# Performance work log

Hardware: AMD Instinct MI355X
Metric: run time of the kernel (lower is better)

## Reference

```python
import jax, jax.numpy as jnp
import numpy as np
import math

NUM_HEADS = 16
KEY_DIM = 64
MODEL_DIM = 1024
NEG_INF = -1000000000.0


def _get_slopes(n):
    def pow2_slopes(n):
        start = 2 ** (-2 ** (-(math.log2(n) - 3)))
        return [start * start ** i for i in range(n)]
    if math.log2(n).is_integer():
        s = pow2_slopes(n)
    else:
        c = 2 ** math.floor(math.log2(n))
        s = pow2_slopes(c) + pow2_slopes(2 * c)[0::2][: n - c]
    return jnp.asarray(s, dtype=jnp.float32)


def setup_inputs() -> dict:
    key = jax.random.key(0)
    ks = jax.random.split(key, 11)
    B, S, D = 4, 2048, MODEL_DIM
    P = NUM_HEADS * KEY_DIM
    sd = 1.0 / math.sqrt(D)
    return {
        "query": jax.random.normal(ks[0], (B, S, D), jnp.float32),
        "key": jax.random.normal(ks[1], (B, S, D), jnp.float32),
        "value": jax.random.normal(ks[2], (B, S, D), jnp.float32),
        "Wq": jax.random.normal(ks[3], (D, P), jnp.float32) * sd,
        "bq": jnp.zeros((P,), jnp.float32),
        "Wk": jax.random.normal(ks[4], (D, P), jnp.float32) * sd,
        "bk": jnp.zeros((P,), jnp.float32),
        "Wv": jax.random.normal(ks[5], (D, P), jnp.float32) * sd,
        "bv": jnp.zeros((P,), jnp.float32),
        "Wo": jax.random.normal(ks[6], (P, D), jnp.float32) * (1.0 / math.sqrt(P)),
        "bo": jnp.zeros((D,), jnp.float32),
    }


def reference(query, key, value, Wq, bq, Wk, bk, Wv, bv, Wo, bo):
    B, S, _ = query.shape
    H, Kd = NUM_HEADS, KEY_DIM

    def split_heads(x):  # [B,S,H*Kd] -> [B,H,S,Kd]
        return x.reshape(B, S, H, Kd).transpose(0, 2, 1, 3)

    q = split_heads(query @ Wq + bq)
    k = split_heads(key @ Wk + bk)
    v = split_heads(value @ Wv + bv)

    logits = jnp.einsum("bhqd,bhkd->bhqk", q, k) / jnp.sqrt(jnp.float32(Kd))

    i = jnp.arange(S)[:, None]
    j = jnp.arange(S)[None, :]
    causal = jnp.where(i >= j, 0.0, NEG_INF).astype(jnp.float32)  # [S,S]
    rel = (i - j).astype(jnp.float32)  # [S,S]
    slopes = _get_slopes(H)  # [H]
    alibi = slopes[:, None, None] * rel  # [H,S,S]
    logits = logits + causal[None, None, :, :] + alibi[None, :, :, :]

    weights = jax.nn.softmax(logits, axis=-1)
    attn = jnp.einsum("bhqk,bhkd->bhqd", weights, v)
    concat = attn.transpose(0, 2, 1, 3).reshape(B, S, H * Kd)
    return concat @ Wo + bo
```

## Files before the change

kernel.cpp:

```cpp
#include <hip/hip_runtime.h>

#define B_ 4
#define S_ 2048
#define D_ 1024
#define H_ 16
#define KD_ 64
#define P_ 1024
#define M_ (B_*S_)

typedef unsigned short u16;
typedef unsigned int u32;
typedef __attribute__((ext_vector_type(4))) float f32x4;
typedef __attribute__((ext_vector_type(8))) __bf16 bf16x8;

__device__ __forceinline__ u16 f2bf(float f) {
  u32 x = __float_as_uint(f);
  return (u16)((x + 0x7fffu + ((x >> 16) & 1u)) >> 16);
}

__device__ __forceinline__ void gl_lds16(const u16* g, u16* l) {
  __builtin_amdgcn_global_load_lds((__attribute__((address_space(1))) void*)g,
                                   (__attribute__((address_space(3))) void*)l, 16, 0, 0);
}

__device__ __forceinline__ u32 pkbf(float a, float b) {
  return __builtin_amdgcn_perm(__float_as_uint(b) + 0x8000u,
                               __float_as_uint(a) + 0x8000u, 0x07060302u);
}

__global__ void cvt3_kernel(const float* __restrict__ q, const float* __restrict__ k,
                            const float* __restrict__ v,
                            u16* __restrict__ Xq, u16* __restrict__ Xk, u16* __restrict__ Xv) {
  const int z = blockIdx.y;
  const float* in = z == 0 ? q : z == 1 ? k : v;
  u16* out = z == 0 ? Xq : z == 1 ? Xk : Xv;
  int i = blockIdx.x * 256 + threadIdx.x;
  float4 vv = ((const float4*)in)[i];
  ((u32*)out)[i*2+0] = (u32)f2bf(vv.x) | ((u32)f2bf(vv.y) << 16);
  ((u32*)out)[i*2+1] = (u32)f2bf(vv.z) | ((u32)f2bf(vv.w) << 16);
}

__global__ void transpose_cvt4(const float* __restrict__ Wq, const float* __restrict__ Wk,
                               const float* __restrict__ Wv, const float* __restrict__ Wo,
                               u16* __restrict__ WqT, u16* __restrict__ WkT,
                               u16* __restrict__ WvT, u16* __restrict__ WoT) {
  const int z = blockIdx.z;
  const float* in = z == 0 ? Wq : z == 1 ? Wk : z == 2 ? Wv : Wo;
  u16* out = z == 0 ? WqT : z == 1 ? WkT : z == 2 ? WvT : WoT;
  __shared__ float tile[32][33];
  int bx = blockIdx.x * 32, by = blockIdx.y * 32;
  int tx = threadIdx.x, ty = threadIdx.y;
  #pragma unroll
  for (int kk = 0; kk < 4; ++kk)
    tile[ty + kk*8][tx] = in[(by + ty + kk*8) * 1024 + bx + tx];
  __syncthreads();
  #pragma unroll
  for (int kk = 0; kk < 4; ++kk)
    out[(bx + ty + kk*8) * 1024 + by + tx] = f2bf(tile[tx][ty + kk*8]);
}

__global__ __launch_bounds__(256) void gemm_qkv(
    const u16* __restrict__ Xq, const u16* __restrict__ Xk, const u16* __restrict__ Xv,
    const u16* __restrict__ WqT, const u16* __restrict__ WkT, const u16* __restrict__ WvT,
    const float* __restrict__ bq, const float* __restrict__ bk, const float* __restrict__ bv,
    u16* __restrict__ Qb, u16* __restrict__ Kb, u16* __restrict__ Vt)
{
  constexpr int K = 1024, N = 1024, BK = 32;
  const int z = blockIdx.z;
  const u16* A  = z == 0 ? Xq  : z == 1 ? Xk  : Xv;
  const u16* Bt = z == 0 ? WqT : z == 1 ? WkT : WvT;
  const float* bias = z == 0 ? bq : z == 1 ? bk : bv;

  __shared__ alignas(16) u16 As[128*BK];
  __shared__ alignas(16) u16 Bs[128*BK];
  const int tid = threadIdx.x;
  const int w = tid >> 6, l = tid & 63;
  const int quad = l >> 4, l16 = l & 15;
  const int wm = (w >> 1) * 64, wn = (w & 1) * 64;
  const long mBase = (long)blockIdx.x * 128;
  const int  nBase = blockIdx.y * 128;

  f32x4 acc[4][4] = {};
  const int off0 = w*1024 + l*16;

  for (int kb = 0; kb < K/BK; ++kb) {
    __syncthreads();
    #pragma unroll
    for (int p = 0; p < 2; ++p) {
      int off = p*4096 + off0;
      int row = off >> 6;
      int cb  = off & 63;
      const u16* ga = A  + (mBase + row)*K + kb*BK + (cb >> 1);
      const u16* gb = Bt + ((long)(nBase + row))*K + kb*BK + (cb >> 1);
      gl_lds16(ga, (u16*)((char*)As + p*4096 + w*1024));
      gl_lds16(gb, (u16*)((char*)Bs + p*4096 + w*1024));
    }
    __syncthreads();
    bf16x8 af[4], bf[4];
    #pragma unroll
    for (int i = 0; i < 4; ++i) af[i] = *(const bf16x8*)&As[(wm + i*16 + l16)*BK + quad*8];
    #pragma unroll
    for (int j = 0; j < 4; ++j) bf[j] = *(const bf16x8*)&Bs[(wn + j*16 + l16)*BK + quad*8];
    #pragma unroll
    for (int i = 0; i < 4; ++i)
      #pragma unroll
      for (int j = 0; j < 4; ++j)
        acc[i][j] = __builtin_amdgcn_mfma_f32_16x16x32_bf16(af[i], bf[j], acc[i][j], 0, 0, 0);
  }

  if (z < 2) {
    u16* Cout = z == 0 ? Qb : Kb;
    #pragma unroll
    for (int i = 0; i < 4; ++i)
      #pragma unroll
      for (int j = 0; j < 4; ++j)
        #pragma unroll
        for (int r = 0; r < 4; ++r) {
          long row = mBase + wm + i*16 + quad*4 + r;
          int  col = nBase + wn + j*16 + l16;
          Cout[row*N + col] = f2bf(acc[i][j][r] + bias[col]);
        }
  } else {
    #pragma unroll
    for (int i = 0; i < 4; ++i)
      #pragma unroll
      for (int j = 0; j < 4; ++j) {
        int  col  = nBase + wn + j*16 + l16;
        long row0 = mBase + wm + i*16 + quad*4;
        int  bb = (int)(row0 >> 11);
        int  ss = (int)(row0 & 2047);
        float bcol = bias[col];
        float v0 = acc[i][j][0] + bcol, v1 = acc[i][j][1] + bcol;
        float v2 = acc[i][j][2] + bcol, v3 = acc[i][j][3] + bcol;
        uint2 pk;
        pk.x = (u32)f2bf(v0) | ((u32)f2bf(v1) << 16);
        pk.y = (u32)f2bf(v2) | ((u32)f2bf(v3) << 16);
        *(uint2*)&Vt[((long)(bb*16) * 64 + col) * 2048 + ss] = pk;
      }
  }
}

__global__ __launch_bounds__(256) void gemm_out(const u16* __restrict__ A,
                                                const u16* __restrict__ Bt,
                                                const float* __restrict__ bias,
                                                float* __restrict__ Cout)
{
  constexpr int K = 1024, N = 1024, BK = 32;
  __shared__ alignas(16) u16 As[128*BK];
  __shared__ alignas(16) u16 Bs[128*BK];
  const int tid = threadIdx.x;
  const int w = tid >> 6, l = tid & 63;
  const int quad = l >> 4, l16 = l & 15;
  const int wm = (w >> 1) * 64, wn = (w & 1) * 64;
  const long mBase = (long)blockIdx.x * 128;
  const int  nBase = blockIdx.y * 128;

  f32x4 acc[4][4] = {};
  const int off0 = w*1024 + l*16;

  for (int kb = 0; kb < K/BK; ++kb) {
    __syncthreads();
    #pragma unroll
    for (int p = 0; p < 2; ++p) {
      int off = p*4096 + off0;
      int row = off >> 6;
      int cb  = off & 63;
      const u16* ga = A  + (mBase + row)*K + kb*BK + (cb >> 1);
      const u16* gb = Bt + ((long)(nBase + row))*K + kb*BK + (cb >> 1);
      gl_lds16(ga, (u16*)((char*)As + p*4096 + w*1024));
      gl_lds16(gb, (u16*)((char*)Bs + p*4096 + w*1024));
    }
    __syncthreads();
    bf16x8 af[4], bf[4];
    #pragma unroll
    for (int i = 0; i < 4; ++i) af[i] = *(const bf16x8*)&As[(wm + i*16 + l16)*BK + quad*8];
    #pragma unroll
    for (int j = 0; j < 4; ++j) bf[j] = *(const bf16x8*)&Bs[(wn + j*16 + l16)*BK + quad*8];
    #pragma unroll
    for (int i = 0; i < 4; ++i)
      #pragma unroll
      for (int j = 0; j < 4; ++j)
        acc[i][j] = __builtin_amdgcn_mfma_f32_16x16x32_bf16(af[i], bf[j], acc[i][j], 0, 0, 0);
  }

  #pragma unroll
  for (int i = 0; i < 4; ++i)
    #pragma unroll
    for (int j = 0; j < 4; ++j)
      #pragma unroll
      for (int r = 0; r < 4; ++r) {
        long row = mBase + wm + i*16 + quad*4 + r;
        int  col = nBase + wn + j*16 + l16;
        Cout[row*N + col] = acc[i][j][r] + bias[col];
      }
}

#define PST 136
__global__ __launch_bounds__(64, 3) void attn_kernel(const u16* __restrict__ Qb,
                                                     const u16* __restrict__ Kb,
                                                     const u16* __restrict__ Vt,
                                                     u16* __restrict__ Ob)
{
  const int n = blockIdx.x;
  const int qt = 15 - (n >> 8);
  const int r8 = n & 255;
  const int b = r8 >> 6, h = (r8 >> 2) & 15, w = r8 & 3;
  const int l = threadIdx.x;
  const int quad = l >> 4, l16 = l & 15;
  const float LOG2E = 1.44269504089f;
  const float slope = exp2f(-0.5f * (float)(h + 1));
  const float c1  = 0.125f * LOG2E;
  const float sl2 = slope * LOG2E;

  __shared__ alignas(16) u16 Ps[2][16][PST];

  const int q0 = qt*128 + w*32;
  const u16* Qp = Qb + ((long)(b*S_ + q0))*P_ + h*KD_;
  const u16* Kp = Kb + ((long)(b*S_))*P_ + h*KD_;
  const u16* Vp = Vt + ((long)(b*H_ + h))*KD_*S_;

  bf16x8 qf[2][2];
  #pragma unroll
  for (int i = 0; i < 2; ++i)
    #pragma unroll
    for (int kk = 0; kk < 2; ++kk)
      qf[i][kk] = *(const bf16x8*)&Qp[(long)(i*16 + l16)*P_ + kk*32 + quad*8];

  f32x4 o[2][4] = {};
  float lsum[2] = {0.f, 0.f};
  const float rs1 = sl2, rs2 = 2.f*sl2, rs3 = 3.f*sl2;

  for (int kt = 0; kt < qt; ++kt) {
    const u16* kts = Kp + (long)(kt*128 + l16)*P_;
    #pragma unroll
    for (int jh = 0; jh < 2; ++jh) {
      f32x4 st[2][4];
      #pragma unroll
      for (int jj = 0; jj < 4; ++jj) {
        const int j = jh*4 + jj;
        const u16* kp = kts + (long)(j*16)*P_;
        bf16x8 kf0 = *(const bf16x8*)(kp + quad*8);
        bf16x8 kf1 = *(const bf16x8*)(kp + 32 + quad*8);
        #pragma unroll
        for (int i = 0; i < 2; ++i) {
          f32x4 t = {};
          t = __builtin_amdgcn_mfma_f32_16x16x32_bf16(kf0, qf[i][0], t, 0, 0, 0);
          t = __builtin_amdgcn_mfma_f32_16x16x32_bf16(kf1, qf[i][1], t, 0, 0, 0);
          st[i][jj] = t;
        }
      }
      #pragma unroll
      for (int i = 0; i < 2; ++i)
        #pragma unroll
        for (int jj = 0; jj < 4; ++jj) {
          const int j = jh*4 + jj;
          const float kb  = (float)(kt*128 + j*16 + quad*4);
          const float bij = -sl2 * kb;
          float p0 = __builtin_amdgcn_exp2f(fmaf(st[i][jj][0], c1, bij));
          float p1 = __builtin_amdgcn_exp2f(fmaf(st[i][jj][1], c1, bij) - rs1);
          float p2 = __builtin_amdgcn_exp2f(fmaf(st[i][jj][2], c1, bij) - rs2);
          float p3 = __builtin_amdgcn_exp2f(fmaf(st[i][jj][3], c1, bij) - rs3);
          lsum[i] += (p0 + p1) + (p2 + p3);
          uint2 pk; pk.x = pkbf(p0, p1); pk.y = pkbf(p2, p3);
          *(uint2*)&Ps[i][l16][j*16 + quad*4] = pk;
        }
    }
    #pragma unroll
    for (int ks = 0; ks < 4; ++ks) {
      bf16x8 pb0 = *(const bf16x8*)&Ps[0][l16][ks*32 + quad*8];
      bf16x8 pb1 = *(const bf16x8*)&Ps[1][l16][ks*32 + quad*8];
      #pragma unroll
      for (int jn = 0; jn < 4; ++jn) {
        bf16x8 vf = *(const bf16x8*)&Vp[(long)(jn*16 + l16)*S_ + kt*128 + ks*32 + quad*8];
        o[0][jn] = __builtin_amdgcn_mfma_f32_16x16x32_bf16(vf, pb0, o[0][jn], 0, 0, 0);
        o[1][jn] = __builtin_amdgcn_mfma_f32_16x16x32_bf16(vf, pb1, o[1][jn], 0, 0, 0);
      }
    }
  }

  {
    const int kt = qt;
    const int jmax = 2*w + 2, ksmax = w + 1;
    const u16* kts = Kp + (long)(kt*128 + l16)*P_;
    for (int j = 0; j < jmax; ++j) {
      const u16* kp = kts + (long)(j*16)*P_;
      bf16x8 kf0 = *(const bf16x8*)(kp + quad*8);
      bf16x8 kf1 = *(const bf16x8*)(kp + 32 + quad*8);
      const int kl0 = j*16 + quad*4;
      const float kb  = (float)(kt*128 + kl0);
      #pragma unroll
      for (int i = 0; i < 2; ++i) {
        f32x4 t = {};
        t = __builtin_amdgcn_mfma_f32_16x16x32_bf16(kf0, qf[i][0], t, 0, 0, 0);
        t = __builtin_amdgcn_mfma_f32_16x16x32_bf16(kf1, qf[i][1], t, 0, 0, 0);
        const int ql = w*32 + i*16 + l16;
        const float bij = -sl2 * kb;
        float x0 = fmaf(t[0], c1, bij);
        float x1 = fmaf(t[1], c1, bij) - rs1;
        float x2 = fmaf(t[2], c1, bij) - rs2;
        float x3 = fmaf(t[3], c1, bij) - rs3;
        if (kl0 + 0 > ql) x0 = -1e30f;
        if (kl0 + 1 > ql) x1 = -1e30f;
        if (kl0 + 2 > ql) x2 = -1e30f;
        if (kl0 + 3 > ql) x3 = -1e30f;
        float p0 = __builtin_amdgcn_exp2f(x0);
        float p1 = __builtin_amdgcn_exp2f(x1);
        float p2 = __builtin_amdgcn_exp2f(x2);
        float p3 = __builtin_amdgcn_exp2f(x3);
        lsum[i] += (p0 + p1) + (p2 + p3);
        uint2 pk; pk.x = pkbf(p0, p1); pk.y = pkbf(p2, p3);
        *(uint2*)&Ps[i][l16][j*16 + quad*4] = pk;
      }
    }
    for (int ks = 0; ks < ksmax; ++ks) {
      bf16x8 pb0 = *(const bf16x8*)&Ps[0][l16][ks*32 + quad*8];
      bf16x8 pb1 = *(const bf16x8*)&Ps[1][l16][ks*32 + quad*8];
      #pragma unroll
      for (int jn = 0; jn < 4; ++jn) {
        bf16x8 vf = *(const bf16x8*)&Vp[(long)(jn*16 + l16)*S_ + kt*128 + ks*32 + quad*8];
        o[0][jn] = __builtin_amdgcn_mfma_f32_16x16x32_bf16(vf, pb0, o[0][jn], 0, 0, 0);
        o[1][jn] = __builtin_amdgcn_mfma_f32_16x16x32_bf16(vf, pb1, o[1][jn], 0, 0, 0);
      }
    }
  }

  #pragma unroll
  for (int i = 0; i < 2; ++i) {
    lsum[i] += __shfl_xor(lsum[i], 16, 64);
    lsum[i] += __shfl_xor(lsum[i], 32, 64);
    const float inv = 1.0f / lsum[i];
    #pragma unroll
    for (int jn = 0; jn < 4; ++jn) {
      float v0 = o[i][jn][0] * inv, v1 = o[i][jn][1] * inv;
      float v2 = o[i][jn][2] * inv, v3 = o[i][jn][3] * inv;
      uint2 pk;
      pk.x = (u32)f2bf(v0) | ((u32)f2bf(v1) << 16);
      pk.y = (u32)f2bf(v2) | ((u32)f2bf(v3) << 16);
      *(uint2*)&Ob[((long)(b*S_ + q0 + i*16 + l16))*P_ + h*KD_ + jn*16 + quad*4] = pk;
    }
  }
}

extern "C" void kernel_launch(void* const* d_in, const int* in_sizes, int n_in,
                              void* d_out, int out_size, void* d_ws, size_t ws_size,
                              hipStream_t stream) {
  const float* q  = (const float*)d_in[0];
  const float* k  = (const float*)d_in[1];
  const float* v  = (const float*)d_in[2];
  const float* Wq = (const float*)d_in[3];
  const float* bq = (const float*)d_in[4];
  const float* Wk = (const float*)d_in[5];
  const float* bk = (const float*)d_in[6];
  const float* Wv = (const float*)d_in[7];
  const float* bv = (const float*)d_in[8];
  const float* Wo = (const float*)d_in[9];
  const float* bo = (const float*)d_in[10];

  const size_t X_ELEMS = (size_t)M_ * P_;
  const size_t W_ELEMS = (size_t)D_ * P_;
  u16* ws  = (u16*)d_ws;
  u16* Xq  = ws;
  u16* Xk  = Xq  + X_ELEMS;
  u16* Xv  = Xk  + X_ELEMS;
  u16* WqT = Xv  + X_ELEMS;
  u16* WkT = WqT + W_ELEMS;
  u16* WvT = WkT + W_ELEMS;
  u16* WoT = WvT + W_ELEMS;
  u16* Qb  = WoT + W_ELEMS;
  u16* Kb  = Qb  + X_ELEMS;
  u16* Vt  = Kb  + X_ELEMS;
  u16* Attn = Xq;

  cvt3_kernel<<<dim3((unsigned)(X_ELEMS/4/256), 3), 256, 0, stream>>>(q, k, v, Xq, Xk, Xv);

  transpose_cvt4<<<dim3(32, 32, 4), dim3(32, 8), 0, stream>>>(Wq, Wk, Wv, Wo,
                                                              WqT, WkT, WvT, WoT);

  gemm_qkv<<<dim3(M_/128, P_/128, 3), 256, 0, stream>>>(Xq, Xk, Xv, WqT, WkT, WvT,
                                                        bq, bk, bv, Qb, Kb, Vt);

  attn_kernel<<<dim3(4096), 64, 0, stream>>>(Qb, Kb, Vt, Attn);

  gemm_out<<<dim3(M_/128, P_/128), 256, 0, stream>>>(Attn, WoT, bo, (float*)d_out);
}
```

Measured before the change: 404.8 us.

## Split attention work into balanced pairs with partial-sum combine kernel

The attention kernel now pairs a long causal q-tile with a short one. Each block handles either the first half of the long tile's key range, or the rest of the long tile plus the whole short tile, so every block does roughly equal work. Partial unnormalized outputs and row sums for the long tiles go to a workspace buffer, and a new combine kernel adds them and normalizes. This works without rescaling because the softmax has no running max. The cost is extra global traffic for the partials, plus one more launch. Launch bounds also rise to allow more resident waves.

```diff
diff --git a/kernel.cpp b/kernel.cpp
--- a/kernel.cpp
+++ b/kernel.cpp
@@ -196,41 +196,26 @@
 }
 
 #define PST 136
-__global__ __launch_bounds__(64, 3) void attn_kernel(const u16* __restrict__ Qb,
-                                                     const u16* __restrict__ Kb,
-                                                     const u16* __restrict__ Vt,
-                                                     u16* __restrict__ Ob)
+__device__ __forceinline__ void attn_tiles(
+    const u16* __restrict__ Qp, const u16* __restrict__ Kp, const u16* __restrict__ Vp,
+    int kt0, int ktN, int qt, bool dodiag, int w, int l16, int quad,
+    float sl2, float c1, u16 (*Ps)[16][PST], f32x4 (&o)[2][4], float (&lsum)[2])
 {
-  const int n = blockIdx.x;
-  const int qt = 15 - (n >> 8);
-  const int r8 = n & 255;
-  const int b = r8 >> 6, h = (r8 >> 2) & 15, w = r8 & 3;
-  const int l = threadIdx.x;
-  const int quad = l >> 4, l16 = l & 15;
-  const float LOG2E = 1.44269504089f;
-  const float slope = exp2f(-0.5f * (float)(h + 1));
-  const float c1  = 0.125f * LOG2E;
-  const float sl2 = slope * LOG2E;
-
-  __shared__ alignas(16) u16 Ps[2][16][PST];
-
-  const int q0 = qt*128 + w*32;
-  const u16* Qp = Qb + ((long)(b*S_ + q0))*P_ + h*KD_;
-  const u16* Kp = Kb + ((long)(b*S_))*P_ + h*KD_;
-  const u16* Vp = Vt + ((long)(b*H_ + h))*KD_*S_;
-
+  const float rs1 = sl2, rs2 = 2.f*sl2, rs3 = 3.f*sl2;
   bf16x8 qf[2][2];
   #pragma unroll
   for (int i = 0; i < 2; ++i)
     #pragma unroll
     for (int kk = 0; kk < 2; ++kk)
       qf[i][kk] = *(const bf16x8*)&Qp[(long)(i*16 + l16)*P_ + kk*32 + quad*8];
-
-  f32x4 o[2][4] = {};
-  float lsum[2] = {0.f, 0.f};
-  const float rs1 = sl2, rs2 = 2.f*sl2, rs3 = 3.f*sl2;
-
-  for (int kt = 0; kt < qt; ++kt) {
+  #pragma unroll
+  for (int i = 0; i < 2; ++i) {
+    lsum[i] = 0.f;
+    #pragma unroll
+    for (int jn = 0; jn < 4; ++jn) o[i][jn] = (f32x4){0.f, 0.f, 0.f, 0.f};
+  }
+
+  for (int kt = kt0; kt < ktN; ++kt) {
     const u16* kts = Kp + (long)(kt*128 + l16)*P_;
     #pragma unroll
     for (int jh = 0; jh < 2; ++jh) {
@@ -278,7 +263,7 @@
     }
   }
 
-  {
+  if (dodiag) {
     const int kt = qt;
     const int jmax = 2*w + 2, ksmax = w + 1;
     const u16* kts = Kp + (long)(kt*128 + l16)*P_;
@@ -323,12 +308,107 @@
       }
     }
   }
-
+}
+
+__global__ __launch_bounds__(64, 4) void attn_kernel(const u16* __restrict__ Qb,
+                                                     const u16* __restrict__ Kb,
+                                                     const u16* __restrict__ Vt,
+                                                     u16* __restrict__ Ob,
+                                                     float* __restrict__ Part)
+{
+  __shared__ alignas(16) u16 Ps[2][16][PST];
+  const int n = blockIdx.x;
+  const int p  = n >> 9;
+  const int ab = (n >> 8) & 1;
+  const int r8 = n & 255;
+  const int b = r8 >> 6, h = (r8 >> 2) & 15, w = r8 & 3;
+  const int qt_hi = 15 - p, qt_lo = p;
+  const int l = threadIdx.x;
+  const int quad = l >> 4, l16 = l & 15;
+  const float LOG2E = 1.44269504089f;
+  const float slope = exp2f(-0.5f * (float)(h + 1));
+  const float c1  = 0.125f * LOG2E;
+  const float sl2 = slope * LOG2E;
+
+  const u16* Kp = Kb + ((long)(b*S_))*P_ + h*KD_;
+  const u16* Vp = Vt + ((long)(b*H_ + h))*KD_*S_;
+  const int slot = ((p*4 + w)*4 + b)*16 + h;
+
+  f32x4 o[2][4];
+  float lsum[2];
+
+  if (ab == 0) {
+    const int q0 = qt_hi*128 + w*32;
+    attn_tiles(Qb + ((long)(b*S_ + q0))*P_ + h*KD_, Kp, Vp,
+               0, 8, qt_hi, false, w, l16, quad, sl2, c1, Ps, o, lsum);
+    float* dst = Part + ((long)slot*64 + l)*36;
+    #pragma unroll
+    for (int i = 0; i < 2; ++i)
+      #pragma unroll
+      for (int jn = 0; jn < 4; ++jn)
+        *(f32x4*)(dst + i*16 + jn*4) = o[i][jn];
+    dst[32] = lsum[0]; dst[33] = lsum[1];
+  } else {
+    const int q0 = qt_hi*128 + w*32;
+    attn_tiles(Qb + ((long)(b*S_ + q0))*P_ + h*KD_, Kp, Vp,
+               8, qt_hi, qt_hi, true, w, l16, quad, sl2, c1, Ps, o, lsum);
+    float* dst = Part + ((long)(2048 + slot)*64 + l)*36;
+    #pragma unroll
+    for (int i = 0; i < 2; ++i)
+      #pragma unroll
+      for (int jn = 0; jn < 4; ++jn)
+        *(f32x4*)(dst + i*16 + jn*4) = o[i][jn];
+    dst[32] = lsum[0]; dst[33] = lsum[1];
+
+    const int q0b = qt_lo*128 + w*32;
+    attn_tiles(Qb + ((long)(b*S_ + q0b))*P_ + h*KD_, Kp, Vp,
+               0, qt_lo, qt_lo, true, w, l16, quad, sl2, c1, Ps, o, lsum);
+    #pragma unroll
+    for (int i = 0; i < 2; ++i) {
+      float ls = lsum[i];
+      ls += __shfl_xor(ls, 16, 64);
+      ls += __shfl_xor(ls, 32, 64);
+      const float inv = 1.0f / ls;
+      #pragma unroll
+      for (int jn = 0; jn < 4; ++jn) {
+        float v0 = o[i][jn][0] * inv, v1 = o[i][jn][1] * inv;
+        float v2 = o[i][jn][2] * inv, v3 = o[i][jn][3] * inv;
+        uint2 pk;
+        pk.x = (u32)f2bf(v0) | ((u32)f2bf(v1) << 16);
+        pk.y = (u32)f2bf(v2) | ((u32)f2bf(v3) << 16);
+        *(uint2*)&Ob[((long)(b*S_ + q0b + i*16 + l16))*P_ + h*KD_ + jn*16 + quad*4] = pk;
+      }
+    }
+  }
+}
+
+__global__ __launch_bounds__(64) void combine_kernel(const float* __restrict__ Part,
+                                                     u16* __restrict__ Ob)
+{
+  const int sid = blockIdx.x;
+  const int l = threadIdx.x;
+  const int h = sid & 15, b = (sid >> 4) & 3, w = (sid >> 6) & 3, p = sid >> 8;
+  const int qt = 15 - p;
+  const int q0 = qt*128 + w*32;
+  const int quad = l >> 4, l16 = l & 15;
+  const float* A  = Part + ((long)sid*64 + l)*36;
+  const float* Bp = Part + ((long)(2048 + sid)*64 + l)*36;
+
+  f32x4 o[2][4];
+  float ls[2];
   #pragma unroll
   for (int i = 0; i < 2; ++i) {
-    lsum[i] += __shfl_xor(lsum[i], 16, 64);
-    lsum[i] += __shfl_xor(lsum[i], 32, 64);
-    const float inv = 1.0f / lsum[i];
+    ls[i] = A[32 + i] + Bp[32 + i];
+    #pragma unroll
+    for (int jn = 0; jn < 4; ++jn)
+      o[i][jn] = *(const f32x4*)(A + i*16 + jn*4) + *(const f32x4*)(Bp + i*16 + jn*4);
+  }
+  #pragma unroll
+  for (int i = 0; i < 2; ++i) {
+    float s = ls[i];
+    s += __shfl_xor(s, 16, 64);
+    s += __shfl_xor(s, 32, 64);
+    const float inv = 1.0f / s;
     #pragma unroll
     for (int jn = 0; jn < 4; ++jn) {
       float v0 = o[i][jn][0] * inv, v1 = o[i][jn][1] * inv;
@@ -370,6 +450,7 @@
   u16* Kb  = Qb  + X_ELEMS;
   u16* Vt  = Kb  + X_ELEMS;
   u16* Attn = Xq;
+  float* Part = (float*)Xk;
 
   cvt3_kernel<<<dim3((unsigned)(X_ELEMS/4/256), 3), 256, 0, stream>>>(q, k, v, Xq, Xk, Xv);
 
@@ -379,7 +460,8 @@
   gemm_qkv<<<dim3(M_/128, P_/128, 3), 256, 0, stream>>>(Xq, Xk, Xv, WqT, WkT, WvT,
                                                         bq, bk, bv, Qb, Kb, Vt);
 
-  attn_kernel<<<dim3(4096), 64, 0, stream>>>(Qb, Kb, Vt, Attn);
+  attn_kernel<<<dim3(4096), 64, 0, stream>>>(Qb, Kb, Vt, Attn, Part);
+  combine_kernel<<<dim3(2048), 64, 0, stream>>>(Part, Attn);
 
   gemm_out<<<dim3(M_/128, P_/128), 256, 0, stream>>>(Attn, WoT, bo, (float*)d_out);
 }
```

Result: slower. 421.2 us (+4.1%).
